# Kernel tuning notes

Hardware: AMD Instinct MI355X
Metric: run time of the kernel (lower is better)

The kernel has to match this reference:

```python
import jax, jax.numpy as jnp
import numpy as np

E = 1.0
I = 1.0
P = 1.0
LENGTH = 1.0
N_POINTS = 2_000_000


def _mlp_scalar(x, W1, b1, W2, b2, W3, b3, W4, b4):
    # x: scalar. 1 -> 15 -> 15 -> 15 -> 1 tanh MLP (dropout inactive, training=False).
    h = jnp.tanh(x * W1[0] + b1)          # [15]
    h = jnp.tanh(h @ W2 + b2)             # [15]
    h = jnp.tanh(h @ W3 + b3)             # [15]
    return (h @ W4 + b4)[0]               # scalar w(x)


def _derivs(x_points, W1, b1, W2, b2, W3, b3, W4, b4):
    """Returns [w, w_x, w_xx, w_xxx, w_xxxx], each of shape [N, 1]."""
    f = lambda x: _mlp_scalar(x, W1, b1, W2, b2, W3, b3, W4, b4)
    d1 = jax.grad(f)
    d2 = jax.grad(d1)
    d3 = jax.grad(d2)
    d4 = jax.grad(d3)
    return [jax.vmap(g)(x_points)[:, None] for g in (f, d1, d2, d3, d4)]


def setup_inputs() -> dict:
    key = jax.random.key(0)
    ks = jax.random.split(key, 5)
    d = 15
    # Glorot-ish small init so tanh stays in its active range
    W1 = jax.random.normal(ks[0], (1, d), jnp.float32) * 0.5
    W2 = jax.random.normal(ks[1], (d, d), jnp.float32) * (1.0 / np.sqrt(d))
    W3 = jax.random.normal(ks[2], (d, d), jnp.float32) * (1.0 / np.sqrt(d))
    W4 = jax.random.normal(ks[3], (d, 1), jnp.float32) * (1.0 / np.sqrt(d))
    x = jax.random.uniform(ks[4], (N_POINTS,), jnp.float32) * LENGTH
    return {
        "x": x,
        "W1": W1, "b1": jnp.zeros((d,), jnp.float32),
        "W2": W2, "b2": jnp.zeros((d,), jnp.float32),
        "W3": W3, "b3": jnp.zeros((d,), jnp.float32),
        "W4": W4, "b4": jnp.zeros((1,), jnp.float32),
    }


def reference(x, W1, b1, W2, b2, W3, b3, W4, b4):
    params = (W1, b1, W2, b2, W3, b3, W4, b4)
    x_left = jnp.zeros_like(x)
    x_right = jnp.full_like(x, LENGTH)

    g_field = _derivs(x, *params)
    g_left = _derivs(x_left, *params)
    g_right = _derivs(x_right, *params)

    w_0, w_0_x = g_left[0], g_left[1]
    m_L = g_right[2]
    w_L = g_right[0]
    w_xxxx = g_field[4]

    pde_residual = w_xxxx + P / (E * I)            # [N,1]
    pde_loss = jnp.mean(jnp.square(pde_residual))  # scalar
    left_bc_w_loss = jnp.square(w_0)               # [N,1]
    left_bc_w_x_loss = jnp.square(w_0_x)           # [N,1]
    right_bc_M_loss = jnp.square(m_L)              # [N,1]
    right_bc_w_loss = jnp.square(w_L)              # [N,1]

    loss = pde_loss + left_bc_w_loss + left_bc_w_x_loss + right_bc_M_loss + right_bc_w_loss
    return (loss, pde_loss, left_bc_w_loss, left_bc_w_x_loss, right_bc_M_loss, right_bc_w_loss)
```

## Files before the change

kernel.cpp:

```cpp
#include <hip/hip_runtime.h>
#include <math.h>

#define DH 15
#define NNODES 64
#define M_DEG  63

typedef float v2f __attribute__((ext_vector_type(2)));

__device__ __forceinline__ void tanh_fs(float u0, float& t, float& s,
                                        float& f2, float& f3, float& f4) {
    float e = __builtin_amdgcn_exp2f(u0 * 2.885390081777927f);
    float r = __builtin_amdgcn_rcpf(1.0f + e);
    t = 1.0f - 2.0f * r;
    s = 4.0f * r * (1.0f - r);
    f2 = -2.0f * t * s;
    f3 = s * (4.0f * t * t - 2.0f * s);
    f4 = 8.0f * t * s * (2.0f * s - t * t);
}

__device__ __forceinline__ void tanh_jet(float u0, float u1, float u2,
                                         float u3, float u4, float h[5]) {
    float t, s, f2, f3, f4;
    tanh_fs(u0, t, s, f2, f3, f4);
    float u1s = u1 * u1;
    h[0] = t;
    h[1] = s * u1;
    h[2] = f2 * u1s + s * u2;
    h[3] = f3 * u1s * u1 + 3.0f * f2 * u1 * u2 + s * u3;
    h[4] = f4 * u1s * u1s + 6.0f * f3 * u1s * u2
         + f2 * (3.0f * u2 * u2 + 4.0f * u1 * u3) + s * u4;
}

__device__ __forceinline__ void fill_region(float* __restrict__ p, float c,
                                            size_t n, size_t tid, size_t stride) {
    size_t head = ((16 - ((size_t)p & 15)) & 15) >> 2;
    if (head > n) head = n;
    if (tid < head) p[tid] = c;
    size_t n4 = (n - head) >> 2;
    float4* p4 = reinterpret_cast<float4*>(p + head);
    float4 cv = {c, c, c, c};
    for (size_t i = tid; i < n4; i += stride) p4[i] = cv;
    size_t t = head + (n4 << 2) + tid;
    if (t < n) p[t] = c;
}

__global__ void __launch_bounds__(256)
pinn_main(const float* __restrict__ x,
          const float* __restrict__ W1, const float* __restrict__ b1,
          const float* __restrict__ W2, const float* __restrict__ b2,
          const float* __restrict__ W3, const float* __restrict__ b3,
          const float* __restrict__ W4, const float* __restrict__ b4,
          float* __restrict__ out, float* __restrict__ bcg,
          double* __restrict__ partials, int N) {
    __shared__ float hs[DH][5][NNODES];
    __shared__ alignas(16) float rsh[NNODES];
    __shared__ float C_lds[NNODES];
    __shared__ float bc_lds[10];
    const int tid  = threadIdx.x;
    const int lane = tid & 63;
    const int wq   = tid >> 6;

    float xv;
    if (lane == 0)           xv = 1.0f;
    else if (lane == M_DEG)  xv = 0.0f;
    else xv = 0.5f + 0.5f * __builtin_amdgcn_cosf((float)lane * (1.0f / 126.0f));

#pragma unroll
    for (int jj = 0; jj < 4; ++jj) {
        int j = wq * 4 + jj;
        if (j < DH) {
            float w = W1[j];
            float t, s, f2, f3, f4;
            tanh_fs(fmaf(xv, w, b1[j]), t, s, f2, f3, f4);
            float w2 = w * w;
            hs[j][0][lane] = t;
            hs[j][1][lane] = s * w;
            hs[j][2][lane] = f2 * w2;
            hs[j][3][lane] = f3 * w2 * w;
            hs[j][4][lane] = f4 * w2 * w2;
        }
    }
    __syncthreads();

    const float* Ws[2] = {W2, W3};
    const float* Bs[2] = {b2, b3};
#pragma unroll
    for (int L = 0; L < 2; ++L) {
        const float* W = Ws[L];
        const float* B = Bs[L];
        float u[4][5];
#pragma unroll
        for (int jj = 0; jj < 4; ++jj)
#pragma unroll
            for (int c = 0; c < 5; ++c) u[jj][c] = 0.f;
#pragma unroll
        for (int k = 0; k < DH; ++k) {
            float g0 = hs[k][0][lane], g1 = hs[k][1][lane], g2 = hs[k][2][lane],
                  g3 = hs[k][3][lane], g4 = hs[k][4][lane];
#pragma unroll
            for (int jj = 0; jj < 4; ++jj) {
                int j = wq * 4 + jj;
                float w = (j < DH) ? W[k * DH + j] : 0.f;
                u[jj][0] = fmaf(g0, w, u[jj][0]);
                u[jj][1] = fmaf(g1, w, u[jj][1]);
                u[jj][2] = fmaf(g2, w, u[jj][2]);
                u[jj][3] = fmaf(g3, w, u[jj][3]);
                u[jj][4] = fmaf(g4, w, u[jj][4]);
            }
        }
        __syncthreads();
#pragma unroll
        for (int jj = 0; jj < 4; ++jj) {
            int j = wq * 4 + jj;
            if (j < DH) {
                float hj[5];
                tanh_jet(u[jj][0] + B[j], u[jj][1], u[jj][2], u[jj][3],
                         u[jj][4], hj);
                hs[j][0][lane] = hj[0]; hs[j][1][lane] = hj[1];
                hs[j][2][lane] = hj[2]; hs[j][3][lane] = hj[3];
                hs[j][4][lane] = hj[4];
            }
        }
        __syncthreads();
    }

    if (wq == 0) {
        float o0 = b4[0], o1 = 0.f, o2 = 0.f, o3 = 0.f, o4 = 0.f;
#pragma unroll
        for (int k = 0; k < DH; ++k) {
            float w = W4[k];
            o0 = fmaf(hs[k][0][lane], w, o0);
            o1 = fmaf(hs[k][1][lane], w, o1);
            o2 = fmaf(hs[k][2][lane], w, o2);
            o3 = fmaf(hs[k][3][lane], w, o3);
            o4 = fmaf(hs[k][4][lane], w, o4);
        }
        rsh[lane] = ((lane == 0 || lane == M_DEG) ? 0.5f : 1.0f) * (o4 + 1.0f);
        if (lane == M_DEG) {
            bc_lds[0] = o0; bc_lds[1] = o1; bc_lds[2] = o2;
            bc_lds[3] = o3; bc_lds[4] = o4;
            if (blockIdx.x == 0) {
                bcg[0] = o0; bcg[1] = o1; bcg[2] = o2; bcg[3] = o3; bcg[4] = o4;
            }
        }
        if (lane == 0) {
            bc_lds[5] = o0; bc_lds[6] = o1; bc_lds[7] = o2;
            bc_lds[8] = o3; bc_lds[9] = o4;
            if (blockIdx.x == 0) {
                bcg[5] = o0; bcg[6] = o1; bcg[7] = o2; bcg[8] = o3; bcg[9] = o4;
            }
        }
        __builtin_amdgcn_s_waitcnt(0);

        float rs[NNODES];
#pragma unroll
        for (int i = 0; i < NNODES / 4; ++i) {
            float4 q = *reinterpret_cast<const float4*>(&rsh[4 * i]);
            rs[4*i] = q.x; rs[4*i+1] = q.y; rs[4*i+2] = q.z; rs[4*i+3] = q.w;
        }
        float kstep = (float)lane * (1.0f / 126.0f);
        float ph = 0.f;
        float a0 = 0.f, a1 = 0.f, a2 = 0.f, a3 = 0.f;
#pragma unroll
        for (int jj = 0; jj < NNODES; ++jj) {
            float cv = __builtin_amdgcn_cosf(ph);
            ph += kstep;
            ph = (ph >= 1.0f) ? ph - 1.0f : ph;
            float v = rs[jj] * cv;
            if ((jj & 3) == 0) a0 += v;
            else if ((jj & 3) == 1) a1 += v;
            else if ((jj & 3) == 2) a2 += v;
            else a3 += v;
        }
        float e = ((a0 + a1) + (a2 + a3)) * (2.0f / 63.0f);
        if (lane == 0 || lane == M_DEG) e *= 0.5f;
        C_lds[lane] = e;
    }
    __syncthreads();

    float lbw  = bc_lds[0] * bc_lds[0];
    float lbwx = bc_lds[1] * bc_lds[1];
    float rbM  = bc_lds[7] * bc_lds[7];
    float rbw  = bc_lds[5] * bc_lds[5];
    float e[NNODES];
#pragma unroll
    for (int k = 0; k < NNODES; ++k) {
        int bits = __builtin_amdgcn_readfirstlane(__float_as_int(C_lds[k]));
        e[k] = __int_as_float(bits);
    }

    size_t gtid = (size_t)blockIdx.x * blockDim.x + tid;
    size_t gstride = (size_t)gridDim.x * blockDim.x;

    fill_region(out + (size_t)1 * N + 1, lbw,  (size_t)N, gtid, gstride);
    fill_region(out + (size_t)2 * N + 1, lbwx, (size_t)N, gtid, gstride);
    fill_region(out + (size_t)3 * N + 1, rbM,  (size_t)N, gtid, gstride);
    fill_region(out + (size_t)4 * N + 1, rbw,  (size_t)N, gtid, gstride);

    v2f accA = {0.f, 0.f}, accB = {0.f, 0.f};
    int i0 = (int)gtid;
    int gsz = (int)gstride;
    int n4 = N >> 2;
    const float4* x4 = reinterpret_cast<const float4*>(x);
    for (int i = i0; i < n4; i += gsz) {
        float4 xv4 = x4[i];
        v2f tA = {2.f * xv4.x - 1.f, 2.f * xv4.y - 1.f};
        v2f tB = {2.f * xv4.z - 1.f, 2.f * xv4.w - 1.f};
        v2f t2A = tA + tA, t2B = tB + tB;
        v2f b0A = {0.f, 0.f}, b1A = {0.f, 0.f};
        v2f b0B = {0.f, 0.f}, b1B = {0.f, 0.f};
#pragma unroll
        for (int k = M_DEG; k >= 1; --k) {
            v2f ek = {e[k], e[k]};
            v2f bnA = __builtin_elementwise_fma(t2A, b0A, ek) - b1A;
            b1A = b0A; b0A = bnA;
            v2f bnB = __builtin_elementwise_fma(t2B, b0B, ek) - b1B;
            b1B = b0B; b0B = bnB;
        }
        v2f e0 = {e[0], e[0]};
        v2f rA = __builtin_elementwise_fma(tA, b0A, e0) - b1A;
        v2f rB = __builtin_elementwise_fma(tB, b0B, e0) - b1B;
        accA = __builtin_elementwise_fma(rA, rA, accA);
        accB = __builtin_elementwise_fma(rB, rB, accB);
    }
    float accs = (accA.x + accA.y) + (accB.x + accB.y);
    for (int i = (n4 << 2) + i0; i < N; i += gsz) {
        float t = 2.f * x[i] - 1.f, t2 = t + t;
        float b0 = 0.f, b1 = 0.f;
#pragma unroll
        for (int k = M_DEG; k >= 1; --k) {
            float bn = fmaf(t2, b0, e[k]) - b1;
            b1 = b0; b0 = bn;
        }
        float r = fmaf(t, b0, e[0]) - b1;
        accs = fmaf(r, r, accs);
    }

    double a = (double)accs;
#pragma unroll
    for (int off = 32; off > 0; off >>= 1) a += __shfl_down(a, off, 64);
    __shared__ double red[4];
    if ((tid & 63) == 0) red[tid >> 6] = a;
    __syncthreads();
    if (tid == 0) partials[blockIdx.x] = red[0] + red[1] + red[2] + red[3];
}

__global__ void __launch_bounds__(256)
pinn_loss(const double* __restrict__ partials, int nparts,
          const float* __restrict__ bc, float* __restrict__ out, int N) {
    int tid = threadIdx.x;
    double a = 0.0;
    for (int i = tid; i < nparts; i += 256) a += partials[i];
#pragma unroll
    for (int off = 32; off > 0; off >>= 1) a += __shfl_down(a, off, 64);
    __shared__ double red[4];
    if ((tid & 63) == 0) red[tid >> 6] = a;
    __syncthreads();
    double total = red[0] + red[1] + red[2] + red[3];
    float pdef = (float)(total / (double)N);
    float lbw  = bc[0] * bc[0];
    float lbwx = bc[1] * bc[1];
    float rbM  = bc[7] * bc[7];
    float rbw  = bc[5] * bc[5];
    float loss = pdef + lbw + lbwx + rbM + rbw;

    size_t gtid = (size_t)blockIdx.x * blockDim.x + tid;
    size_t gstride = (size_t)gridDim.x * blockDim.x;
    fill_region(out, loss, (size_t)N, gtid, gstride);
    if (blockIdx.x == 0 && tid == 0) out[N] = pdef;
}

extern "C" void kernel_launch(void* const* d_in, const int* in_sizes, int n_in,
                              void* d_out, int out_size, void* d_ws, size_t ws_size,
                              hipStream_t stream) {
    const float* x  = (const float*)d_in[0];
    const float* W1 = (const float*)d_in[1];
    const float* b1 = (const float*)d_in[2];
    const float* W2 = (const float*)d_in[3];
    const float* b2 = (const float*)d_in[4];
    const float* W3 = (const float*)d_in[5];
    const float* b3 = (const float*)d_in[6];
    const float* W4 = (const float*)d_in[7];
    const float* b4 = (const float*)d_in[8];
    float* out = (float*)d_out;
    int N = in_sizes[0];

    float*  bc       = (float*)((char*)d_ws + 256);
    double* partials = (double*)((char*)d_ws + 1024);

    int NB = 512;
    size_t need = 1024 + (size_t)NB * 8;
    if (ws_size < need) {
        NB = (int)((ws_size > 1024 + 8) ? (ws_size - 1024) / 8 : 1);
        if (NB < 1) NB = 1;
        if (NB > 512) NB = 512;
    }

    hipLaunchKernelGGL(pinn_main, dim3(NB), dim3(256), 0, stream,
                       x, W1, b1, W2, b2, W3, b3, W4, b4,
                       out, bc, partials, N);
    int gx = (N / 4 + 255) / 256;
    if (gx > 512) gx = 512;
    if (gx < 1) gx = 1;
    hipLaunchKernelGGL(pinn_loss, dim3(gx), dim3(256), 0, stream,
                       partials, NB, bc, out, N);
}
```

Before: 29.56 us.

## Move BC fills to second kernel and prefetch x before Chebyshev setup

```diff
diff --git a/kernel.cpp b/kernel.cpp
--- a/kernel.cpp
+++ b/kernel.cpp
@@ -45,20 +45,31 @@
 }
 
 __global__ void __launch_bounds__(256)
-pinn_main(const float* __restrict__ x,
-          const float* __restrict__ W1, const float* __restrict__ b1,
-          const float* __restrict__ W2, const float* __restrict__ b2,
-          const float* __restrict__ W3, const float* __restrict__ b3,
-          const float* __restrict__ W4, const float* __restrict__ b4,
-          float* __restrict__ out, float* __restrict__ bcg,
-          double* __restrict__ partials, int N) {
+pinn_pde(const float* __restrict__ x,
+         const float* __restrict__ W1, const float* __restrict__ b1,
+         const float* __restrict__ W2, const float* __restrict__ b2,
+         const float* __restrict__ W3, const float* __restrict__ b3,
+         const float* __restrict__ W4, const float* __restrict__ b4,
+         float* __restrict__ bcg, double* __restrict__ partials, int N) {
     __shared__ float hs[DH][5][NNODES];
     __shared__ alignas(16) float rsh[NNODES];
     __shared__ float C_lds[NNODES];
-    __shared__ float bc_lds[10];
     const int tid  = threadIdx.x;
     const int lane = tid & 63;
     const int wq   = tid >> 6;
+
+    int i0 = blockIdx.x * blockDim.x + tid;
+    int gsz = gridDim.x * blockDim.x;
+    int n4 = N >> 2;
+    const float4* x4 = reinterpret_cast<const float4*>(x);
+    float4 px[4];
+    bool pv[4];
+#pragma unroll
+    for (int m = 0; m < 4; ++m) {
+        int ii = i0 + m * gsz;
+        pv[m] = (ii < n4);
+        px[m] = pv[m] ? x4[ii] : float4{0.f, 0.f, 0.f, 0.f};
+    }
 
     float xv;
     if (lane == 0)           xv = 1.0f;
@@ -136,17 +147,11 @@
             o4 = fmaf(hs[k][4][lane], w, o4);
         }
         rsh[lane] = ((lane == 0 || lane == M_DEG) ? 0.5f : 1.0f) * (o4 + 1.0f);
-        if (lane == M_DEG) {
-            bc_lds[0] = o0; bc_lds[1] = o1; bc_lds[2] = o2;
-            bc_lds[3] = o3; bc_lds[4] = o4;
-            if (blockIdx.x == 0) {
+        if (blockIdx.x == 0) {
+            if (lane == M_DEG) {
                 bcg[0] = o0; bcg[1] = o1; bcg[2] = o2; bcg[3] = o3; bcg[4] = o4;
             }
-        }
-        if (lane == 0) {
-            bc_lds[5] = o0; bc_lds[6] = o1; bc_lds[7] = o2;
-            bc_lds[8] = o3; bc_lds[9] = o4;
-            if (blockIdx.x == 0) {
+            if (lane == 0) {
                 bcg[5] = o0; bcg[6] = o1; bcg[7] = o2; bcg[8] = o3; bcg[9] = o4;
             }
         }
@@ -178,10 +183,6 @@
     }
     __syncthreads();
 
-    float lbw  = bc_lds[0] * bc_lds[0];
-    float lbwx = bc_lds[1] * bc_lds[1];
-    float rbM  = bc_lds[7] * bc_lds[7];
-    float rbw  = bc_lds[5] * bc_lds[5];
     float e[NNODES];
 #pragma unroll
     for (int k = 0; k < NNODES; ++k) {
@@ -189,20 +190,32 @@
         e[k] = __int_as_float(bits);
     }
 
-    size_t gtid = (size_t)blockIdx.x * blockDim.x + tid;
-    size_t gstride = (size_t)gridDim.x * blockDim.x;
-
-    fill_region(out + (size_t)1 * N + 1, lbw,  (size_t)N, gtid, gstride);
-    fill_region(out + (size_t)2 * N + 1, lbwx, (size_t)N, gtid, gstride);
-    fill_region(out + (size_t)3 * N + 1, rbM,  (size_t)N, gtid, gstride);
-    fill_region(out + (size_t)4 * N + 1, rbw,  (size_t)N, gtid, gstride);
-
     v2f accA = {0.f, 0.f}, accB = {0.f, 0.f};
-    int i0 = (int)gtid;
-    int gsz = (int)gstride;
-    int n4 = N >> 2;
-    const float4* x4 = reinterpret_cast<const float4*>(x);
-    for (int i = i0; i < n4; i += gsz) {
+#pragma unroll
+    for (int m = 0; m < 4; ++m) {
+        if (pv[m]) {
+            float4 xv4 = px[m];
+            v2f tA = {2.f * xv4.x - 1.f, 2.f * xv4.y - 1.f};
+            v2f tB = {2.f * xv4.z - 1.f, 2.f * xv4.w - 1.f};
+            v2f t2A = tA + tA, t2B = tB + tB;
+            v2f b0A = {0.f, 0.f}, b1A = {0.f, 0.f};
+            v2f b0B = {0.f, 0.f}, b1B = {0.f, 0.f};
+#pragma unroll
+            for (int k = M_DEG; k >= 1; --k) {
+                v2f ek = {e[k], e[k]};
+                v2f bnA = __builtin_elementwise_fma(t2A, b0A, ek) - b1A;
+                b1A = b0A; b0A = bnA;
+                v2f bnB = __builtin_elementwise_fma(t2B, b0B, ek) - b1B;
+                b1B = b0B; b0B = bnB;
+            }
+            v2f e0 = {e[0], e[0]};
+            v2f rA = __builtin_elementwise_fma(tA, b0A, e0) - b1A;
+            v2f rB = __builtin_elementwise_fma(tB, b0B, e0) - b1B;
+            accA = __builtin_elementwise_fma(rA, rA, accA);
+            accB = __builtin_elementwise_fma(rB, rB, accB);
+        }
+    }
+    for (int i = i0 + 4 * gsz; i < n4; i += gsz) {
         float4 xv4 = x4[i];
         v2f tA = {2.f * xv4.x - 1.f, 2.f * xv4.y - 1.f};
         v2f tB = {2.f * xv4.z - 1.f, 2.f * xv4.w - 1.f};
@@ -246,9 +259,22 @@
 }
 
 __global__ void __launch_bounds__(256)
-pinn_loss(const double* __restrict__ partials, int nparts,
-          const float* __restrict__ bc, float* __restrict__ out, int N) {
+pinn_out(const double* __restrict__ partials, int nparts,
+         const float* __restrict__ bc, float* __restrict__ out, int N) {
     int tid = threadIdx.x;
+    float c0 = bc[0], c1 = bc[1], c7 = bc[7], c5 = bc[5];
+    float lbw  = c0 * c0;
+    float lbwx = c1 * c1;
+    float rbM  = c7 * c7;
+    float rbw  = c5 * c5;
+
+    size_t gtid = (size_t)blockIdx.x * blockDim.x + tid;
+    size_t gstride = (size_t)gridDim.x * blockDim.x;
+    fill_region(out + (size_t)1 * N + 1, lbw,  (size_t)N, gtid, gstride);
+    fill_region(out + (size_t)2 * N + 1, lbwx, (size_t)N, gtid, gstride);
+    fill_region(out + (size_t)3 * N + 1, rbM,  (size_t)N, gtid, gstride);
+    fill_region(out + (size_t)4 * N + 1, rbw,  (size_t)N, gtid, gstride);
+
     double a = 0.0;
     for (int i = tid; i < nparts; i += 256) a += partials[i];
 #pragma unroll
@@ -258,14 +284,8 @@
     __syncthreads();
     double total = red[0] + red[1] + red[2] + red[3];
     float pdef = (float)(total / (double)N);
-    float lbw  = bc[0] * bc[0];
-    float lbwx = bc[1] * bc[1];
-    float rbM  = bc[7] * bc[7];
-    float rbw  = bc[5] * bc[5];
     float loss = pdef + lbw + lbwx + rbM + rbw;
 
-    size_t gtid = (size_t)blockIdx.x * blockDim.x + tid;
-    size_t gstride = (size_t)gridDim.x * blockDim.x;
     fill_region(out, loss, (size_t)N, gtid, gstride);
     if (blockIdx.x == 0 && tid == 0) out[N] = pdef;
 }
@@ -296,12 +316,8 @@
         if (NB > 512) NB = 512;
     }
 
-    hipLaunchKernelGGL(pinn_main, dim3(NB), dim3(256), 0, stream,
-                       x, W1, b1, W2, b2, W3, b3, W4, b4,
-                       out, bc, partials, N);
-    int gx = (N / 4 + 255) / 256;
-    if (gx > 512) gx = 512;
-    if (gx < 1) gx = 1;
-    hipLaunchKernelGGL(pinn_loss, dim3(gx), dim3(256), 0, stream,
+    hipLaunchKernelGGL(pinn_pde, dim3(NB), dim3(256), 0, stream,
+                       x, W1, b1, W2, b2, W3, b3, W4, b4, bc, partials, N);
+    hipLaunchKernelGGL(pinn_out, dim3(512), dim3(256), 0, stream,
                        partials, NB, bc, out, N);
 }
```

New measurement: 28.32 us. -4.2%, faster.
